# Kernel tuning notes

Hardware: AMD Instinct MI355X
Metric: run time of the kernel (lower is better)

The kernel has to match this reference:

```python
import jax, jax.numpy as jnp
import numpy as np


def setup_inputs() -> dict:
    key = jax.random.key(0)
    k1, k2 = jax.random.split(key)
    b, n, d = 8, 4096, 128
    qk = jax.random.normal(k1, (b, n, d), dtype=jnp.float32)
    v = jax.random.normal(k2, (b, n, d), dtype=jnp.float32)
    return {"qk": qk, "v": v}


def reference(qk, v):
    # qk: [b, n, d] shared query/key tensor; v: [b, n, d]
    b, n, d = qk.shape
    # keys = L2-normalized qk (F.normalize eps=1e-12); queries = raw qk
    k = qk / jnp.maximum(jnp.linalg.norm(qk, axis=-1, keepdims=True), 1e-12)
    scores = jnp.einsum('bie,bje->bij', qk, k) * (d ** -0.5)  # [b, n, n]
    # mask self-attention on the diagonal with -inf
    eye = jnp.eye(n, dtype=bool)
    scores = jnp.where(eye[None, :, :], -jnp.inf, scores)
    attn = jax.nn.softmax(scores, axis=-1)
    out = jnp.einsum('bij,bje->bie', attn, v)  # [b, n, d]
    return out
```

## Files before the change

### kernel.cpp

```cpp
#include <hip/hip_runtime.h>
#include <hip/hip_bf16.h>
#include <stdint.h>

#define BATCH 8
#define SEQN  4096
#define DIM   128
#define KVB   64
#define HALF  2048
#define NTH   (HALF / KVB)
#define QW    32
#define QB    128
#define EP_S  34

typedef __attribute__((ext_vector_type(16))) float f32x16;
typedef __bf16 bf16x8 __attribute__((ext_vector_type(8)));

#define GAS __attribute__((address_space(1)))
#define LAS __attribute__((address_space(3)))

__device__ __forceinline__ ushort f2b(float x) {
  union { float f; uint32_t u; } a; a.f = x;
  uint32_t r = a.u + 0x7fffu + ((a.u >> 16) & 1u);
  return (ushort)(r >> 16);
}
__device__ __forceinline__ uint32_t pkbf(float a, float b) {
  union { __bf16 h[2]; uint32_t u; } x;
  x.h[0] = (__bf16)a; x.h[1] = (__bf16)b;
  return x.u;
}

__global__ __launch_bounds__(256) void prep_kernel(
    const float* __restrict__ qk, ushort* __restrict__ qb, ushort* __restrict__ kb) {
  int row  = blockIdx.x * 4 + (threadIdx.x >> 6);
  int ln   = threadIdx.x & 63;
  size_t roff = (size_t)row * DIM;
  float2 q2 = *(const float2*)(qk + roff + ln * 2);
  float ss = q2.x * q2.x + q2.y * q2.y;
  #pragma unroll
  for (int m = 32; m; m >>= 1) ss += __shfl_xor(ss, m, 64);
  float r = 1.0f / fmaxf(sqrtf(ss), 1e-12f);
  const float SC = 1.44269504088896340736f / 11.313708498984761f;
  float rs = r * SC;
  *(uint32_t*)(qb + roff + ln * 2) =
      (uint32_t)f2b(q2.x) | ((uint32_t)f2b(q2.y) << 16);
  int ch = ln >> 2;
  int pos = ((ch ^ (row & 7)) << 3) + (ln & 3) * 2;
  *(uint32_t*)(kb + roff + pos) =
      (uint32_t)f2b(q2.x * rs) | ((uint32_t)f2b(q2.y * rs) << 16);
}

__global__ __launch_bounds__(256) void vtrans_kernel(
    const float* __restrict__ v, ushort* __restrict__ vt) {
  __shared__ ushort t[64][136];
  int tile = blockIdx.x;
  const float* src = v + (size_t)tile * KVB * DIM;
  int tid = threadIdx.x;
  #pragma unroll
  for (int i = 0; i < 8; ++i) {
    int n = tid + 256 * i;
    int r = n >> 5, c4 = n & 31;
    float4 f = *(const float4*)(src + r * DIM + 4 * c4);
    *(uint32_t*)&t[r][4 * c4]     = pkbf(f.x, f.y);
    *(uint32_t*)&t[r][4 * c4 + 2] = pkbf(f.z, f.w);
  }
  __syncthreads();
  ushort* dst = vt + (size_t)tile * 8192;
  #pragma unroll
  for (int i = 0; i < 4; ++i) {
    int n = tid + 256 * i;
    int d = n >> 3, c = n & 7;
    ushort tmp[8];
    #pragma unroll
    for (int j = 0; j < 8; ++j) tmp[j] = t[8 * c + j][d];
    *(int4*)(dst + d * 64 + ((c ^ (d & 7)) << 3)) = *(int4*)tmp;
  }
}

__global__ __launch_bounds__(512, 2) void attn_kernel(
    const ushort* __restrict__ qb, const ushort* __restrict__ kb,
    const ushort* __restrict__ vt, float* __restrict__ out) {
  __shared__ ushort lds_all[65536];

  const int tid = threadIdx.x;
  const int w  = tid >> 6;
  const int l  = tid & 63;
  const int ql = l & 31;
  const int hi = l >> 5;
  const int qc = w & 3;
  const int hf = w >> 2;

  const int bidx  = blockIdx.x;
  const int batch = bidx & 7;
  const int qt    = bidx >> 3;
  const int q0W   = qt * QB + qc * QW;
  const size_t base = (size_t)batch * SEQN * DIM;

  const ushort* kb_b = kb + base;
  const ushort* vt_b = vt + base;

  bf16x8 qf[8];
  {
    const ushort* qp = qb + base + (size_t)(q0W + ql) * DIM + hi * 8;
    #pragma unroll
    for (int kc = 0; kc < 8; ++kc) qf[kc] = *(const bf16x8*)(qp + kc * 16);
  }

  f32x16 o[4];
  #pragma unroll
  for (int db = 0; db < 4; ++db)
    #pragma unroll
    for (int r = 0; r < 16; ++r) o[db][r] = 0.f;
  float m = -INFINITY, lsum = 0.f;

  const int tT  = w >> 1;
  const int sub = w & 1;

#define STAGE(bsel, kt_) do {                                                  \
    const ushort* srcs_;                                                       \
    if      (tT == 0) srcs_ = kb_b + (size_t)((kt_) * KVB) * DIM;              \
    else if (tT == 1) srcs_ = kb_b + (size_t)(HALF + (kt_) * KVB) * DIM;       \
    else if (tT == 2) srcs_ = vt_b + (size_t)(kt_) * 8192;                     \
    else              srcs_ = vt_b + (size_t)(32 + (kt_)) * 8192;              \
    ushort* dbase_ = lds_all + (bsel) * 32768 + tT * 8192 + sub * 4096;        \
    const ushort* sbase_ = srcs_ + sub * 4096 + l * 8;                         \
    _Pragma("unroll")                                                          \
    for (int i_ = 0; i_ < 8; ++i_)                                             \
      __builtin_amdgcn_global_load_lds((const GAS uint32_t*)(sbase_ + i_*512), \
                                       (LAS uint32_t*)(dbase_ + i_*512),       \
                                       16, 0, 0);                              \
  } while (0)

  STAGE(0, 0);
  asm volatile("s_waitcnt vmcnt(0)" ::: "memory");
  __syncthreads();

  int buf = 0;
  for (int kt = 0; kt < NTH; ++kt) {
    if (kt + 1 < NTH) STAGE(buf ^ 1, kt + 1);
    const int kv0 = hf * HALF + kt * KVB;
    const ushort* kbase = lds_all + buf * 32768 + hf * 8192;
    const ushort* vbase = lds_all + buf * 32768 + 16384 + hf * 8192;

    f32x16 st[2];
    __builtin_amdgcn_s_setprio(1);
    #pragma unroll
    for (int n2 = 0; n2 < 2; ++n2) {
      #pragma unroll
      for (int r = 0; r < 16; ++r) st[n2][r] = 0.f;
      #pragma unroll
      for (int kc = 0; kc < 8; ++kc) {
        const int row = 32 * n2 + ql;
        const int chunk = (2 * kc + hi) ^ (ql & 7);
        const bf16x8 kf = *(const bf16x8*)(kbase + row * 128 + (chunk << 3));
        st[n2] = __builtin_amdgcn_mfma_f32_32x32x16_bf16(kf, qf[kc], st[n2], 0, 0, 0);
      }
    }
    __builtin_amdgcn_s_setprio(0);

    if ((q0W & ~(KVB - 1)) == kv0) {
      const int dloc = q0W + ql - kv0;
      #pragma unroll
      for (int n2 = 0; n2 < 2; ++n2)
        #pragma unroll
        for (int r = 0; r < 16; ++r) {
          int crow = (r & 3) + 8 * (r >> 2) + 4 * hi + 32 * n2;
          if (crow == dloc) st[n2][r] = -1e30f;
        }
    }

    float pm = st[0][0];
    #pragma unroll
    for (int r = 1; r < 16; ++r) pm = fmaxf(pm, st[0][r]);
    #pragma unroll
    for (int r = 0; r < 16; ++r) pm = fmaxf(pm, st[1][r]);
    pm = fmaxf(pm, __shfl_xor(pm, 32, 64));
    if (__any(pm > m + 8.0f)) {
      float mn = fmaxf(m, pm);
      float sc = exp2f(m - mn);
      m = mn; lsum *= sc;
      #pragma unroll
      for (int db = 0; db < 4; ++db)
        #pragma unroll
        for (int r = 0; r < 16; ++r) o[db][r] *= sc;
    }
    float rs = 0.f;
    #pragma unroll
    for (int n2 = 0; n2 < 2; ++n2)
      #pragma unroll
      for (int r = 0; r < 16; ++r) {
        float p = exp2f(st[n2][r] - m);
        st[n2][r] = p;
        rs += p;
      }
    rs += __shfl_xor(rs, 32, 64);
    lsum += rs;

    uint32_t ww[2][4][2];
    #pragma unroll
    for (int n2 = 0; n2 < 2; ++n2)
      #pragma unroll
      for (int q = 0; q < 4; ++q) {
        ww[n2][q][0] = pkbf(st[n2][4 * q + 0], st[n2][4 * q + 1]);
        ww[n2][q][1] = pkbf(st[n2][4 * q + 2], st[n2][4 * q + 3]);
      }
    bf16x8 pa[4];
    #pragma unroll
    for (int ks = 0; ks < 4; ++ks) {
      const int n2 = ks >> 1, kk = ks & 1;
      uint32_t ow0 = hi ? ww[n2][2*kk+1][0] : ww[n2][2*kk][0];
      uint32_t ow1 = hi ? ww[n2][2*kk+1][1] : ww[n2][2*kk][1];
      uint32_t sv0 = hi ? ww[n2][2*kk][0]   : ww[n2][2*kk+1][0];
      uint32_t sv1 = hi ? ww[n2][2*kk][1]   : ww[n2][2*kk+1][1];
      uint32_t rv0 = (uint32_t)__shfl_xor((int)sv0, 32, 64);
      uint32_t rv1 = (uint32_t)__shfl_xor((int)sv1, 32, 64);
      union { uint32_t u[4]; bf16x8 v; } pb;
      pb.u[0] = hi ? rv0 : ow0;
      pb.u[1] = hi ? rv1 : ow1;
      pb.u[2] = hi ? ow0 : rv0;
      pb.u[3] = hi ? ow1 : rv1;
      pa[ks] = pb.v;
    }

    __builtin_amdgcn_s_setprio(1);
    #pragma unroll
    for (int db = 0; db < 4; ++db)
      #pragma unroll
      for (int ks = 0; ks < 4; ++ks) {
        const int row = 32 * db + ql;
        const int chunk = (2 * ks + hi) ^ (ql & 7);
        const bf16x8 vv = *(const bf16x8*)(vbase + row * 64 + (chunk << 3));
        o[db] = __builtin_amdgcn_mfma_f32_32x32x16_bf16(vv, pa[ks], o[db], 0, 0, 0);
      }
    __builtin_amdgcn_s_setprio(0);

    asm volatile("s_waitcnt vmcnt(0)" ::: "memory");
    __syncthreads();
    buf ^= 1;
  }
#undef STAGE

  float* fl = (float*)lds_all;
  if (hi == 0) { fl[w * 64 + ql] = m; fl[w * 64 + 32 + ql] = lsum; }
  __syncthreads();
  const int pw = w ^ 4;
  float m_o = fl[pw * 64 + ql];
  float l_o = fl[pw * 64 + 32 + ql];
  float M = fmaxf(m, m_o);
  float sc_self = exp2f(m - M);
  float l_tot = lsum * sc_self + l_o * exp2f(m_o - M);

  float* oreg = (float*)lds_all + 1024 + qc * 4096;
  if (hf == 1) {
    #pragma unroll
    for (int db = 0; db < 4; ++db)
      #pragma unroll
      for (int r = 0; r < 16; ++r) {
        int crow = (r & 3) + 8 * (r >> 2) + 4 * hi;
        oreg[crow * 128 + 32 * db + ql] = o[db][r] * sc_self;
      }
  }
  __syncthreads();
  if (hf == 0) {
    const float inv = 1.0f / l_tot;
    #pragma unroll
    for (int db = 0; db < 4; ++db)
      #pragma unroll
      for (int r = 0; r < 16; ++r) {
        int crow = (r & 3) + 8 * (r >> 2) + 4 * hi;
        o[db][r] = (o[db][r] * sc_self + oreg[crow * 128 + 32 * db + ql]) * inv;
      }
    float* epw = (float*)lds_all + 17408 + w * (QW * EP_S);
    float* outb = out + base;
    #pragma unroll
    for (int db = 0; db < 4; ++db) {
      #pragma unroll
      for (int rr = 0; rr < 8; ++rr) {
        const int r0 = 2 * rr;
        const int crow = (r0 & 3) + 8 * (r0 >> 2) + 4 * hi;
        *(float2*)(epw + ql * EP_S + crow) = make_float2(o[db][r0], o[db][r0 + 1]);
      }
      __builtin_amdgcn_s_waitcnt(0);
      #pragma unroll
      for (int s = 0; s < 8; ++s) {
        const int row = 4 * s + (l >> 4);
        const int c2  = l & 15;
        float2 v2 = *(const float2*)(epw + row * EP_S + 2 * c2);
        *(float2*)(outb + (size_t)(q0W + row) * DIM + 32 * db + 2 * c2) = v2;
      }
      __builtin_amdgcn_s_waitcnt(0);
    }
  }
}

extern "C" void kernel_launch(void* const* d_in, const int* in_sizes, int n_in,
                              void* d_out, int out_size, void* d_ws, size_t ws_size,
                              hipStream_t stream) {
  (void)in_sizes; (void)n_in; (void)out_size; (void)ws_size;
  const float* qk = (const float*)d_in[0];
  const float* v  = (const float*)d_in[1];
  float* out = (float*)d_out;
  size_t nelem = (size_t)BATCH * SEQN * DIM;
  ushort* qb = (ushort*)d_ws;
  ushort* kb = qb + nelem;
  ushort* vt = kb + nelem;
  prep_kernel<<<BATCH * SEQN / 4, 256, 0, stream>>>(qk, qb, kb);
  vtrans_kernel<<<BATCH * (SEQN / KVB), 256, 0, stream>>>(v, vt);
  attn_kernel<<<BATCH * (SEQN / QB), 512, 0, stream>>>(qb, kb, vt, out);
}
```

Baseline: 120.5 us.

## Pre-swizzle Q/K/V into MFMA fragment order and split KV four ways

The prep kernels now write Q, K and V in 32-row tiles already laid out in MFMA fragment order. The attention kernel can then load K fragments straight from global memory and keep only Q and V in LDS. The attention block shrinks to 64 queries with eight waves: two query chunks times four KV quarters. Each inner step handles a 32-key tile, LDS use drops, and occupancy is raised to four blocks, with a four-way merge of the softmax partials at the end. In exchange there are more blocks and more partial-result merges, and K is read from global memory on every step with no reuse through LDS.

```diff
diff --git a/kernel.cpp b/kernel.cpp
--- a/kernel.cpp
+++ b/kernel.cpp
@@ -5,12 +5,6 @@
 #define BATCH 8
 #define SEQN  4096
 #define DIM   128
-#define KVB   64
-#define HALF  2048
-#define NTH   (HALF / KVB)
-#define QW    32
-#define QB    128
-#define EP_S  34
 
 typedef __attribute__((ext_vector_type(16))) float f32x16;
 typedef __bf16 bf16x8 __attribute__((ext_vector_type(8)));
@@ -29,81 +23,120 @@
   return x.u;
 }
 
-__global__ __launch_bounds__(256) void prep_kernel(
-    const float* __restrict__ qk, ushort* __restrict__ qb, ushort* __restrict__ kb) {
-  int row  = blockIdx.x * 4 + (threadIdx.x >> 6);
-  int ln   = threadIdx.x & 63;
-  size_t roff = (size_t)row * DIM;
-  float2 q2 = *(const float2*)(qk + roff + ln * 2);
-  float ss = q2.x * q2.x + q2.y * q2.y;
-  #pragma unroll
-  for (int m = 32; m; m >>= 1) ss += __shfl_xor(ss, m, 64);
-  float r = 1.0f / fmaxf(sqrtf(ss), 1e-12f);
+
+__global__ __launch_bounds__(256) void prep_qk(
+    const float* __restrict__ qk, ushort* __restrict__ qfb, ushort* __restrict__ kfb) {
+  __shared__ ushort qt_l[32 * 136];
+  __shared__ ushort kt_l[32 * 136];
+  const int g = blockIdx.x;
+  const int t = threadIdx.x;
+  const int r = t >> 3, s = t & 7;
+  const float* src = qk + (size_t)g * 4096 + r * 128 + s * 16;
+  float x[16];
+  #pragma unroll
+  for (int i = 0; i < 4; ++i) {
+    float4 f = ((const float4*)src)[i];
+    x[4*i] = f.x; x[4*i+1] = f.y; x[4*i+2] = f.z; x[4*i+3] = f.w;
+  }
+  float ss = 0.f;
+  #pragma unroll
+  for (int i = 0; i < 16; ++i) ss += x[i] * x[i];
+  ss += __shfl_xor(ss, 1, 64);
+  ss += __shfl_xor(ss, 2, 64);
+  ss += __shfl_xor(ss, 4, 64);
+  float rn = 1.0f / fmaxf(sqrtf(ss), 1e-12f);
   const float SC = 1.44269504088896340736f / 11.313708498984761f;
-  float rs = r * SC;
-  *(uint32_t*)(qb + roff + ln * 2) =
-      (uint32_t)f2b(q2.x) | ((uint32_t)f2b(q2.y) << 16);
-  int ch = ln >> 2;
-  int pos = ((ch ^ (row & 7)) << 3) + (ln & 3) * 2;
-  *(uint32_t*)(kb + roff + pos) =
-      (uint32_t)f2b(q2.x * rs) | ((uint32_t)f2b(q2.y * rs) << 16);
-}
-
-__global__ __launch_bounds__(256) void vtrans_kernel(
-    const float* __restrict__ v, ushort* __restrict__ vt) {
-  __shared__ ushort t[64][136];
-  int tile = blockIdx.x;
-  const float* src = v + (size_t)tile * KVB * DIM;
-  int tid = threadIdx.x;
-  #pragma unroll
-  for (int i = 0; i < 8; ++i) {
-    int n = tid + 256 * i;
-    int r = n >> 5, c4 = n & 31;
-    float4 f = *(const float4*)(src + r * DIM + 4 * c4);
-    *(uint32_t*)&t[r][4 * c4]     = pkbf(f.x, f.y);
-    *(uint32_t*)&t[r][4 * c4 + 2] = pkbf(f.z, f.w);
-  }
-  __syncthreads();
-  ushort* dst = vt + (size_t)tile * 8192;
+  float rs = rn * SC;
+  #pragma unroll
+  for (int j = 0; j < 16; ++j) {
+    qt_l[r * 136 + s * 16 + j] = f2b(x[j]);
+    kt_l[r * 136 + s * 16 + j] = f2b(x[j] * rs);
+  }
+  __syncthreads();
+  #pragma unroll
+  for (int p = 0; p < 2; ++p) {
+    int sl = t + 256 * p;
+    int qli = sl & 31, grp = sl >> 5;
+    union { ushort u[8]; int4 v; } tq, tk;
+    #pragma unroll
+    for (int j = 0; j < 8; ++j) {
+      tq.u[j] = qt_l[qli * 136 + grp * 8 + j];
+      tk.u[j] = kt_l[qli * 136 + grp * 8 + j];
+    }
+    *(int4*)(qfb + (size_t)g * 4096 + sl * 8) = tq.v;
+    *(int4*)(kfb + (size_t)g * 4096 + sl * 8) = tk.v;
+  }
+}
+
+__global__ __launch_bounds__(256) void prep_v(
+    const float* __restrict__ v, ushort* __restrict__ vfb) {
+  __shared__ ushort vt_l[32 * 136];
+  const int g = blockIdx.x;
+  const int t = threadIdx.x;
+  const int r = t >> 3, s = t & 7;
+  const float* src = v + (size_t)g * 4096 + r * 128 + s * 16;
   #pragma unroll
   for (int i = 0; i < 4; ++i) {
-    int n = tid + 256 * i;
-    int d = n >> 3, c = n & 7;
-    ushort tmp[8];
-    #pragma unroll
-    for (int j = 0; j < 8; ++j) tmp[j] = t[8 * c + j][d];
-    *(int4*)(dst + d * 64 + ((c ^ (d & 7)) << 3)) = *(int4*)tmp;
-  }
-}
-
-__global__ __launch_bounds__(512, 2) void attn_kernel(
-    const ushort* __restrict__ qb, const ushort* __restrict__ kb,
-    const ushort* __restrict__ vt, float* __restrict__ out) {
-  __shared__ ushort lds_all[65536];
+    float4 f = ((const float4*)src)[i];
+    vt_l[r * 136 + s * 16 + 4*i]     = f2b(f.x);
+    vt_l[r * 136 + s * 16 + 4*i + 1] = f2b(f.y);
+    vt_l[r * 136 + s * 16 + 4*i + 2] = f2b(f.z);
+    vt_l[r * 136 + s * 16 + 4*i + 3] = f2b(f.w);
+  }
+  __syncthreads();
+  #pragma unroll
+  for (int p = 0; p < 2; ++p) {
+    int sl = t + 256 * p;
+    int qli = sl & 31, grp = sl >> 5;
+    int db = grp >> 2, ks = (grp >> 1) & 1, hh = grp & 1;
+    union { ushort u[8]; int4 v; } tv;
+    #pragma unroll
+    for (int j = 0; j < 8; ++j)
+      tv.u[j] = vt_l[(16 * ks + 8 * hh + j) * 136 + 32 * db + qli];
+    *(int4*)(vfb + (size_t)g * 4096 + sl * 8) = tv.v;
+  }
+}
+
+__global__ __launch_bounds__(512, 4) void attn_kernel(
+    const ushort* __restrict__ qfb, const ushort* __restrict__ kfb,
+    const ushort* __restrict__ vfb, float* __restrict__ out) {
+  __shared__ ushort lds[40960];
 
   const int tid = threadIdx.x;
   const int w  = tid >> 6;
   const int l  = tid & 63;
   const int ql = l & 31;
   const int hi = l >> 5;
-  const int qc = w & 3;
-  const int hf = w >> 2;
+  const int qc = w & 1;
+  const int hf = w >> 1;
 
   const int bidx  = blockIdx.x;
   const int batch = bidx & 7;
   const int qt    = bidx >> 3;
-  const int q0W   = qt * QB + qc * QW;
-  const size_t base = (size_t)batch * SEQN * DIM;
-
-  const ushort* kb_b = kb + base;
-  const ushort* vt_b = vt + base;
-
-  bf16x8 qf[8];
+  const int q0    = qt * 64 + qc * 32;
+  const size_t qpb   = ((size_t)batch * 128 + qt * 2) * 4096;
+  const size_t kvch0 = (size_t)batch * 128 + hf * 32;
+
   {
-    const ushort* qp = qb + base + (size_t)(q0W + ql) * DIM + hi * 8;
-    #pragma unroll
-    for (int kc = 0; kc < 8; ++kc) qf[kc] = *(const bf16x8*)(qp + kc * 16);
-  }
+    const ushort* qsrc = qfb + qpb + w * 1024 + l * 8;
+    #pragma unroll
+    for (int i = 0; i < 2; ++i)
+      __builtin_amdgcn_global_load_lds((const GAS uint32_t*)(qsrc + i * 512),
+          (LAS uint32_t*)(lds + (65536 + w * 2048 + i * 1024) / 2), 16, 0, 0);
+  }
+
+#define STAGE(bsel, t_) do {                                                   \
+    const ushort* vsrc_ = vfb + (kvch0 + (t_)) * 4096 + qc * 2048 + l * 8;     \
+    _Pragma("unroll")                                                          \
+    for (int i_ = 0; i_ < 4; ++i_)                                             \
+      __builtin_amdgcn_global_load_lds((const GAS uint32_t*)(vsrc_ + i_ * 512),\
+          (LAS uint32_t*)(lds + ((bsel) * 32768 + hf * 8192 + qc * 4096 +      \
+                                 i_ * 1024) / 2), 16, 0, 0);                   \
+  } while (0)
+
+  STAGE(0, 0);
+  asm volatile("s_waitcnt vmcnt(0)" ::: "memory");
+  __syncthreads();
 
   f32x16 o[4];
   #pragma unroll
@@ -112,105 +145,72 @@
     for (int r = 0; r < 16; ++r) o[db][r] = 0.f;
   float m = -INFINITY, lsum = 0.f;
 
-  const int tT  = w >> 1;
-  const int sub = w & 1;
-
-#define STAGE(bsel, kt_) do {                                                  \
-    const ushort* srcs_;                                                       \
-    if      (tT == 0) srcs_ = kb_b + (size_t)((kt_) * KVB) * DIM;              \
-    else if (tT == 1) srcs_ = kb_b + (size_t)(HALF + (kt_) * KVB) * DIM;       \
-    else if (tT == 2) srcs_ = vt_b + (size_t)(kt_) * 8192;                     \
-    else              srcs_ = vt_b + (size_t)(32 + (kt_)) * 8192;              \
-    ushort* dbase_ = lds_all + (bsel) * 32768 + tT * 8192 + sub * 4096;        \
-    const ushort* sbase_ = srcs_ + sub * 4096 + l * 8;                         \
-    _Pragma("unroll")                                                          \
-    for (int i_ = 0; i_ < 8; ++i_)                                             \
-      __builtin_amdgcn_global_load_lds((const GAS uint32_t*)(sbase_ + i_*512), \
-                                       (LAS uint32_t*)(dbase_ + i_*512),       \
-                                       16, 0, 0);                              \
-  } while (0)
-
-  STAGE(0, 0);
-  asm volatile("s_waitcnt vmcnt(0)" ::: "memory");
-  __syncthreads();
-
   int buf = 0;
-  for (int kt = 0; kt < NTH; ++kt) {
-    if (kt + 1 < NTH) STAGE(buf ^ 1, kt + 1);
-    const int kv0 = hf * HALF + kt * KVB;
-    const ushort* kbase = lds_all + buf * 32768 + hf * 8192;
-    const ushort* vbase = lds_all + buf * 32768 + 16384 + hf * 8192;
-
-    f32x16 st[2];
+  for (int t = 0; t < 32; ++t) {
+    if (t + 1 < 32) STAGE(buf ^ 1, t + 1);
+
+    const ushort* kt_p = kfb + (kvch0 + t) * 4096 + l * 8;
+    bf16x8 kf[8];
+    #pragma unroll
+    for (int kc = 0; kc < 8; ++kc) kf[kc] = *(const bf16x8*)(kt_p + kc * 512);
+
+    f32x16 st;
+    #pragma unroll
+    for (int r = 0; r < 16; ++r) st[r] = 0.f;
+    const ushort* qlp = lds + (32768 + qc * 4096) + l * 8;
     __builtin_amdgcn_s_setprio(1);
     #pragma unroll
-    for (int n2 = 0; n2 < 2; ++n2) {
-      #pragma unroll
-      for (int r = 0; r < 16; ++r) st[n2][r] = 0.f;
-      #pragma unroll
-      for (int kc = 0; kc < 8; ++kc) {
-        const int row = 32 * n2 + ql;
-        const int chunk = (2 * kc + hi) ^ (ql & 7);
-        const bf16x8 kf = *(const bf16x8*)(kbase + row * 128 + (chunk << 3));
-        st[n2] = __builtin_amdgcn_mfma_f32_32x32x16_bf16(kf, qf[kc], st[n2], 0, 0, 0);
-      }
+    for (int kc = 0; kc < 8; ++kc) {
+      bf16x8 qf = *(const bf16x8*)(qlp + kc * 512);
+      st = __builtin_amdgcn_mfma_f32_32x32x16_bf16(kf[kc], qf, st, 0, 0, 0);
     }
     __builtin_amdgcn_s_setprio(0);
 
-    if ((q0W & ~(KVB - 1)) == kv0) {
-      const int dloc = q0W + ql - kv0;
-      #pragma unroll
-      for (int n2 = 0; n2 < 2; ++n2)
-        #pragma unroll
-        for (int r = 0; r < 16; ++r) {
-          int crow = (r & 3) + 8 * (r >> 2) + 4 * hi + 32 * n2;
-          if (crow == dloc) st[n2][r] = -1e30f;
-        }
-    }
-
-    float pm = st[0][0];
-    #pragma unroll
-    for (int r = 1; r < 16; ++r) pm = fmaxf(pm, st[0][r]);
-    #pragma unroll
-    for (int r = 0; r < 16; ++r) pm = fmaxf(pm, st[1][r]);
+    const int kv0g = hf * 1024 + t * 32;
+    if (kv0g == q0) {
+      #pragma unroll
+      for (int r = 0; r < 16; ++r) {
+        int crow = (r & 3) + 8 * (r >> 2) + 4 * hi;
+        if (crow == ql) st[r] = -1e30f;
+      }
+    }
+
+    float pm = st[0];
+    #pragma unroll
+    for (int r = 1; r < 16; ++r) pm = fmaxf(pm, st[r]);
     pm = fmaxf(pm, __shfl_xor(pm, 32, 64));
     if (__any(pm > m + 8.0f)) {
       float mn = fmaxf(m, pm);
-      float sc = exp2f(m - mn);
-      m = mn; lsum *= sc;
+      float sc0 = exp2f(m - mn);
+      m = mn; lsum *= sc0;
       #pragma unroll
       for (int db = 0; db < 4; ++db)
         #pragma unroll
-        for (int r = 0; r < 16; ++r) o[db][r] *= sc;
-    }
-    float rs = 0.f;
-    #pragma unroll
-    for (int n2 = 0; n2 < 2; ++n2)
-      #pragma unroll
-      for (int r = 0; r < 16; ++r) {
-        float p = exp2f(st[n2][r] - m);
-        st[n2][r] = p;
-        rs += p;
-      }
-    rs += __shfl_xor(rs, 32, 64);
-    lsum += rs;
-
-    uint32_t ww[2][4][2];
-    #pragma unroll
-    for (int n2 = 0; n2 < 2; ++n2)
-      #pragma unroll
-      for (int q = 0; q < 4; ++q) {
-        ww[n2][q][0] = pkbf(st[n2][4 * q + 0], st[n2][4 * q + 1]);
-        ww[n2][q][1] = pkbf(st[n2][4 * q + 2], st[n2][4 * q + 3]);
-      }
-    bf16x8 pa[4];
-    #pragma unroll
-    for (int ks = 0; ks < 4; ++ks) {
-      const int n2 = ks >> 1, kk = ks & 1;
-      uint32_t ow0 = hi ? ww[n2][2*kk+1][0] : ww[n2][2*kk][0];
-      uint32_t ow1 = hi ? ww[n2][2*kk+1][1] : ww[n2][2*kk][1];
-      uint32_t sv0 = hi ? ww[n2][2*kk][0]   : ww[n2][2*kk+1][0];
-      uint32_t sv1 = hi ? ww[n2][2*kk][1]   : ww[n2][2*kk+1][1];
+        for (int r = 0; r < 16; ++r) o[db][r] *= sc0;
+    }
+    float rs_ = 0.f;
+    #pragma unroll
+    for (int r = 0; r < 16; ++r) {
+      float p = exp2f(st[r] - m);
+      st[r] = p;
+      rs_ += p;
+    }
+    rs_ += __shfl_xor(rs_, 32, 64);
+    lsum += rs_;
+
+    uint32_t ww[4][2];
+    #pragma unroll
+    for (int q4 = 0; q4 < 4; ++q4) {
+      ww[q4][0] = pkbf(st[4 * q4 + 0], st[4 * q4 + 1]);
+      ww[q4][1] = pkbf(st[4 * q4 + 2], st[4 * q4 + 3]);
+    }
+    bf16x8 pa[2];
+    #pragma unroll
+    for (int ks = 0; ks < 2; ++ks) {
+      uint32_t ow0 = hi ? ww[2*ks+1][0] : ww[2*ks][0];
+      uint32_t ow1 = hi ? ww[2*ks+1][1] : ww[2*ks][1];
+      uint32_t sv0 = hi ? ww[2*ks][0]   : ww[2*ks+1][0];
+      uint32_t sv1 = hi ? ww[2*ks][1]   : ww[2*ks+1][1];
       uint32_t rv0 = (uint32_t)__shfl_xor((int)sv0, 32, 64);
       uint32_t rv1 = (uint32_t)__shfl_xor((int)sv1, 32, 64);
       union { uint32_t u[4]; bf16x8 v; } pb;
@@ -221,14 +221,13 @@
       pa[ks] = pb.v;
     }
 
+    const ushort* vlp = lds + (buf * 16384 + hf * 4096) + l * 8;
     __builtin_amdgcn_s_setprio(1);
     #pragma unroll
     for (int db = 0; db < 4; ++db)
       #pragma unroll
-      for (int ks = 0; ks < 4; ++ks) {
-        const int row = 32 * db + ql;
-        const int chunk = (2 * ks + hi) ^ (ql & 7);
-        const bf16x8 vv = *(const bf16x8*)(vbase + row * 64 + (chunk << 3));
+      for (int ks = 0; ks < 2; ++ks) {
+        bf16x8 vv = *(const bf16x8*)(vlp + (db * 4 + ks * 2) * 256);
         o[db] = __builtin_amdgcn_mfma_f32_32x32x16_bf16(vv, pa[ks], o[db], 0, 0, 0);
       }
     __builtin_amdgcn_s_setprio(0);
@@ -239,53 +238,71 @@
   }
 #undef STAGE
 
-  float* fl = (float*)lds_all;
-  if (hi == 0) { fl[w * 64 + ql] = m; fl[w * 64 + 32 + ql] = lsum; }
-  __syncthreads();
-  const int pw = w ^ 4;
-  float m_o = fl[pw * 64 + ql];
-  float l_o = fl[pw * 64 + 32 + ql];
-  float M = fmaxf(m, m_o);
-  float sc_self = exp2f(m - M);
-  float l_tot = lsum * sc_self + l_o * exp2f(m_o - M);
-
-  float* oreg = (float*)lds_all + 1024 + qc * 4096;
-  if (hf == 1) {
+  float* flds = (float*)lds;
+  if (hi == 0) { flds[w * 64 + ql] = m; flds[w * 64 + 32 + ql] = lsum; }
+  __syncthreads();
+  float M = -INFINITY, mi4[4];
+  #pragma unroll
+  for (int i = 0; i < 4; ++i) {
+    mi4[i] = flds[(qc + 2 * i) * 64 + ql];
+    M = fmaxf(M, mi4[i]);
+  }
+  float L = 0.f;
+  #pragma unroll
+  for (int i = 0; i < 4; ++i)
+    L += flds[(qc + 2 * i) * 64 + 32 + ql] * exp2f(mi4[i] - M);
+  const float sc = exp2f(m - M);
+  float* oA = flds + 512 + qc * 8704;
+  float* oB = oA + 4352;
+
+  if (hf == 3 || hf == 1) {
+    float* dst = (hf == 3) ? oA : oB;
     #pragma unroll
     for (int db = 0; db < 4; ++db)
       #pragma unroll
       for (int r = 0; r < 16; ++r) {
         int crow = (r & 3) + 8 * (r >> 2) + 4 * hi;
-        oreg[crow * 128 + 32 * db + ql] = o[db][r] * sc_self;
-      }
-  }
-  __syncthreads();
-  if (hf == 0) {
-    const float inv = 1.0f / l_tot;
+        dst[(32 * db + crow) * 34 + ql] = o[db][r] * sc;
+      }
+  }
+  __syncthreads();
+  if (hf == 2 || hf == 0) {
+    float* dst = (hf == 2) ? oA : oB;
     #pragma unroll
     for (int db = 0; db < 4; ++db)
       #pragma unroll
       for (int r = 0; r < 16; ++r) {
         int crow = (r & 3) + 8 * (r >> 2) + 4 * hi;
-        o[db][r] = (o[db][r] * sc_self + oreg[crow * 128 + 32 * db + ql]) * inv;
-      }
-    float* epw = (float*)lds_all + 17408 + w * (QW * EP_S);
-    float* outb = out + base;
+        dst[(32 * db + crow) * 34 + ql] += o[db][r] * sc;
+      }
+  }
+  __syncthreads();
+  if (hf == 0) {
+    const float inv = 1.0f / L;
+    float* epw = flds + 17920 + qc * 1088;
+    float* outb = out + (size_t)batch * SEQN * DIM;
     #pragma unroll
     for (int db = 0; db < 4; ++db) {
+      float fin[16];
+      #pragma unroll
+      for (int r = 0; r < 16; ++r) {
+        int crow = (r & 3) + 8 * (r >> 2) + 4 * hi;
+        int idx = (32 * db + crow) * 34 + ql;
+        fin[r] = (oA[idx] + oB[idx]) * inv;
+      }
       #pragma unroll
       for (int rr = 0; rr < 8; ++rr) {
-        const int r0 = 2 * rr;
-        const int crow = (r0 & 3) + 8 * (r0 >> 2) + 4 * hi;
-        *(float2*)(epw + ql * EP_S + crow) = make_float2(o[db][r0], o[db][r0 + 1]);
+        int r0 = 2 * rr;
+        int crow = (r0 & 3) + 8 * (r0 >> 2) + 4 * hi;
+        *(float2*)(epw + ql * 34 + crow) = make_float2(fin[r0], fin[r0 + 1]);
       }
       __builtin_amdgcn_s_waitcnt(0);
       #pragma unroll
-      for (int s = 0; s < 8; ++s) {
-        const int row = 4 * s + (l >> 4);
-        const int c2  = l & 15;
-        float2 v2 = *(const float2*)(epw + row * EP_S + 2 * c2);
-        *(float2*)(outb + (size_t)(q0W + row) * DIM + 32 * db + 2 * c2) = v2;
+      for (int s2 = 0; s2 < 8; ++s2) {
+        int row = 4 * s2 + (l >> 4);
+        int c2  = l & 15;
+        float2 v2 = *(const float2*)(epw + row * 34 + 2 * c2);
+        *(float2*)(outb + (size_t)(q0 + row) * DIM + 32 * db + 2 * c2) = v2;
       }
       __builtin_amdgcn_s_waitcnt(0);
     }
@@ -300,10 +317,10 @@
   const float* v  = (const float*)d_in[1];
   float* out = (float*)d_out;
   size_t nelem = (size_t)BATCH * SEQN * DIM;
-  ushort* qb = (ushort*)d_ws;
-  ushort* kb = qb + nelem;
-  ushort* vt = kb + nelem;
-  prep_kernel<<<BATCH * SEQN / 4, 256, 0, stream>>>(qk, qb, kb);
-  vtrans_kernel<<<BATCH * (SEQN / KVB), 256, 0, stream>>>(v, vt);
-  attn_kernel<<<BATCH * (SEQN / QB), 512, 0, stream>>>(qb, kb, vt, out);
-}
+  ushort* qfb = (ushort*)d_ws;
+  ushort* kfb = qfb + nelem;
+  ushort* vfb = kfb + nelem;
+  prep_qk<<<BATCH * SEQN / 32, 256, 0, stream>>>(qk, qfb, kfb);
+  prep_v <<<BATCH * SEQN / 32, 256, 0, stream>>>(v, vfb);
+  attn_kernel<<<BATCH * (SEQN / 64), 512, 0, stream>>>(qfb, kfb, vfb, out);
+}
```

New measurement: 128.7 us. 6.8% more time.
